# Kernel optimization log

Measured on AMD Instinct MI355X. Metric: run time of the kernel, lower is better.

Reference implementation:

```python
import jax, jax.numpy as jnp
import numpy as np
from jax import lax

FEAT = 192   # features
GROUP = 3
B, H, W = 16, 64, 64
CIN = 2 * FEAT        # 384, input channels of x
CGATE = 4 * FEAT      # 768, gate channels


def _group_ids(C, g=GROUP):
    # contiguous channel blocks: channel c -> group c*g//C
    return (np.arange(C) * g) // C


def _mask_B(out_c, in_c, kw):
    # PixelRNN mask 'B' for a (1,kw) kernel: left-of-center columns fully
    # connected, center column obeys group rule (out_group >= in_group),
    # right-of-center columns blocked.
    og = _group_ids(out_c)[:, None]
    ig = _group_ids(in_c)[None, :]
    center = (og >= ig).astype(np.float32)  # (out_c, in_c)
    m = np.zeros((out_c, in_c, 1, kw), dtype=np.float32)
    m[:, :, :, : kw // 2] = 1.0
    m[:, :, 0, kw // 2] = center
    return jnp.asarray(m)


def _shuffle(h):
    # (B, 3*4*(F/3), H, W): group-major gate layout -> gate-major group layout
    b, c, hh, ww = h.shape
    return h.reshape(b, GROUP, 4, FEAT // GROUP, hh, ww) \
            .transpose(0, 2, 1, 3, 4, 5).reshape(b, c, hh, ww)


def setup_inputs() -> dict:
    key = jax.random.key(0)
    k1, k2, k3, k4, k5 = jax.random.split(key, 5)
    x = jax.random.normal(k1, (B, CIN, H, W), dtype=jnp.float32)
    w_i2s = jax.random.normal(k2, (CGATE, CIN, 1, 3), dtype=jnp.float32) * 0.02
    w_s2s = jax.random.normal(k3, (CGATE, FEAT, 1, 3), dtype=jnp.float32) * 0.02
    w_skip = jax.random.normal(k4, (CIN, FEAT, 1, 1), dtype=jnp.float32) * 0.05
    b_skip = jax.random.normal(k5, (CIN,), dtype=jnp.float32) * 0.01
    return {"x": x, "w_i2s": w_i2s, "w_s2s": w_s2s,
            "w_skip": w_skip, "b_skip": b_skip}


def reference(x, w_i2s, w_s2s, w_skip, b_skip):
    mask_i2s = _mask_B(CGATE, CIN, 3)
    mask_skip = _mask_B(CIN, FEAT, 1)

    # input-to-state: masked (1,3) conv, 'same' padding on width
    h = lax.conv_general_dilated(
        x, w_i2s * mask_i2s, (1, 1), ((0, 0), (1, 1)),
        dimension_numbers=("NCHW", "OIHW", "NCHW"))
    h = _shuffle(h)                       # (B, 4F, H, W)

    w1 = w_s2s[:, :, 0, :]                # (4F, F, 3) for 1D width conv
    h_rows = h.transpose(2, 0, 1, 3)      # (H, B, 4F, W)

    def step(carry, h_row):
        _h, c = carry                     # each (B, F, W)
        s = lax.conv_general_dilated(
            _h, w1, (1,), ((1, 1),),
            dimension_numbers=("NCW", "OIW", "NCW")) + h_row
        o, f, i, g = jnp.split(jax.nn.sigmoid(s), 4, axis=1)
        c = f * c + i * g
        _h = o * jnp.tanh(c)
        return (_h, c), _h

    init = (jnp.zeros((B, FEAT, W), x.dtype), jnp.zeros((B, FEAT, W), x.dtype))
    _, out_h = lax.scan(step, init, h_rows)   # (H, B, F, W)
    out_h = out_h.transpose(1, 2, 0, 3)       # (B, F, H, W)

    skip = lax.conv_general_dilated(
        out_h, w_skip * mask_skip, (1, 1), ((0, 0), (0, 0)),
        dimension_numbers=("NCHW", "OIHW", "NCHW")) + b_skip[None, :, None, None]
    return x + skip
```

## Files before the change

kernel.cpp:

```cpp
#include <hip/hip_runtime.h>
#include <hip/hip_cooperative_groups.h>
#include <cmath>

#define FEAT  192
#define CINCH 384
#define CGATE 768
#define BATCH 16
#define HH    64
#define WW    64
#define NP    (BATCH*HH*WW)
#define KI2S  768
#define KS2S  576
#define NBLK  192
#define SCANT 512

using bf16   = __bf16;
using bf16x8 = __attribute__((ext_vector_type(8))) __bf16;
using bf16x4 = __attribute__((ext_vector_type(4))) __bf16;
using f32x4  = __attribute__((ext_vector_type(4))) float;
typedef unsigned long long u64;

__device__ __forceinline__ void ic_store64(u64* p, u64 v) {
    __hip_atomic_store(p, v, __ATOMIC_RELAXED, __HIP_MEMORY_SCOPE_AGENT);
}
__device__ __forceinline__ u64 ic_load64(const u64* p) {
    return __hip_atomic_load(p, __ATOMIC_RELAXED, __HIP_MEMORY_SCOPE_AGENT);
}
__device__ __forceinline__ void ic_store32(unsigned* p, unsigned v) {
    __hip_atomic_store(p, v, __ATOMIC_RELAXED, __HIP_MEMORY_SCOPE_AGENT);
}
__device__ __forceinline__ unsigned ic_load32(const unsigned* p) {
    return __hip_atomic_load(p, __ATOMIC_RELAXED, __HIP_MEMORY_SCOPE_AGENT);
}

__device__ __forceinline__ float sigm_fast(float v) {
    return __builtin_amdgcn_rcpf(1.f + __expf(-v));
}
__device__ __forceinline__ float tanh_fast(float v) {
    return 1.f - 2.f * __builtin_amdgcn_rcpf(1.f + __expf(2.f * v));
}

__global__ void pack_weights(const float* __restrict__ wi, const float* __restrict__ ws,
                             const float* __restrict__ wk,
                             bf16* __restrict__ WpA, bf16* __restrict__ WpS,
                             bf16* __restrict__ WpK) {
    int tid = blockIdx.x * 256 + threadIdx.x;
    int stride = gridDim.x * 256;
    for (int idx = tid; idx < CGATE * KI2S; idx += stride) {
        int cp = idx / KI2S, k = idx % KI2S;
        int q = cp / 192, r = cp % 192, g = r / 64, f = r % 64;
        int c = g * 256 + q * 64 + f;
        float v;
        if (k < CINCH) {
            v = wi[(c * CINCH + k) * 3 + 0];
        } else {
            int ic = k - CINCH;
            v = (g >= ic / 128) ? wi[(c * CINCH + ic) * 3 + 1] : 0.f;
        }
        WpA[idx] = (bf16)v;
    }
    for (int idx = tid; idx < CGATE * KS2S; idx += stride) {
        int oc = idx / KS2S, k = idx % KS2S;
        int t = k / FEAT, f = k % FEAT;
        WpS[idx] = (bf16)ws[(oc * FEAT + f) * 3 + t];
    }
    for (int idx = tid; idx < CINCH * FEAT; idx += stride) {
        int co = idx / FEAT, f = idx % FEAT;
        WpK[idx] = (co / 128 >= f / 64) ? (bf16)wk[idx] : (bf16)0.f;
    }
}

__global__ void pack_x(const float* __restrict__ x, bf16* __restrict__ Xp) {
    __shared__ float tile[64][65];
    int b = blockIdx.x >> 6, y = blockIdx.x & 63;
    const float* xb = x + ((size_t)b * CINCH * HH + y) * WW;
    bf16* Xrow = Xp + ((size_t)b * HH * WW + (size_t)y * WW) * KI2S;
    for (int ic0 = 0; ic0 < CINCH; ic0 += 64) {
        for (int rep = 0; rep < 16; ++rep) {
            int idx = rep * 256 + threadIdx.x;
            int i = idx >> 6, w = idx & 63;
            tile[i][w] = xb[(size_t)(ic0 + i) * (HH * WW) + w];
        }
        __syncthreads();
        for (int rep = 0; rep < 16; ++rep) {
            int idx = rep * 256 + threadIdx.x;
            int w = idx >> 6, i = idx & 63;
            Xrow[(size_t)w * KI2S + CINCH + ic0 + i] = (bf16)tile[i][w];
            Xrow[(size_t)w * KI2S + ic0 + i] = (w == 0) ? (bf16)0.f : (bf16)tile[i][w - 1];
        }
        __syncthreads();
    }
}

__global__ __launch_bounds__(256) void gemm_i2s(const bf16* __restrict__ A,
                                                const bf16* __restrict__ B,
                                                bf16* __restrict__ Hout) {
    __shared__ __align__(16) bf16 As[128 * 64];
    __shared__ __align__(16) bf16 Bs[128 * 64];
    const int m0 = blockIdx.y * 128;
    const int p0 = blockIdx.x * 128;
    const int tid = threadIdx.x;
    const int lane = tid & 63, wid = tid >> 6;
    const int quad = lane >> 4, col = lane & 15;
    const int mhalf = (wid & 1) * 64, nhalf = (wid >> 1) * 64;
    f32x4 acc[4][4] = {};
    for (int k0 = 0; k0 < KI2S; k0 += 64) {
        #pragma unroll
        for (int r = 0; r < 4; ++r) {
            int L = r * 256 + tid;
            int row = L >> 3, slot = L & 7;
            int c = slot ^ (row & 7);
            const bf16* srcA = &A[(size_t)(m0 + row) * KI2S + k0 + c * 8];
            const bf16* srcB = &B[(size_t)(p0 + row) * KI2S + k0 + c * 8];
            bf16* dstA = As + (size_t)(r * 256 + wid * 64) * 8;
            bf16* dstB = Bs + (size_t)(r * 256 + wid * 64) * 8;
            __builtin_amdgcn_global_load_lds(
                (const __attribute__((address_space(1))) void*)srcA,
                (__attribute__((address_space(3))) void*)dstA, 16, 0, 0);
            __builtin_amdgcn_global_load_lds(
                (const __attribute__((address_space(1))) void*)srcB,
                (__attribute__((address_space(3))) void*)dstB, 16, 0, 0);
        }
        __syncthreads();
        for (int kk = 0; kk < 2; ++kk) {
            bf16x8 af[4], bfv[4];
            for (int mt = 0; mt < 4; ++mt) {
                int row = mhalf + mt * 16 + col;
                int slot = (kk * 4 + quad) ^ (row & 7);
                af[mt] = *(const bf16x8*)(&As[row * 64 + slot * 8]);
            }
            for (int nt = 0; nt < 4; ++nt) {
                int row = nhalf + nt * 16 + col;
                int slot = (kk * 4 + quad) ^ (row & 7);
                bfv[nt] = *(const bf16x8*)(&Bs[row * 64 + slot * 8]);
            }
            for (int mt = 0; mt < 4; ++mt)
                for (int nt = 0; nt < 4; ++nt)
                    acc[mt][nt] = __builtin_amdgcn_mfma_f32_16x16x32_bf16(
                        af[mt], bfv[nt], acc[mt][nt], 0, 0, 0);
        }
        __syncthreads();
    }
    for (int mt = 0; mt < 4; ++mt)
        for (int nt = 0; nt < 4; ++nt) {
            int m = m0 + mhalf + mt * 16 + quad * 4;
            int p = p0 + nhalf + nt * 16 + col;
            for (int r = 0; r < 4; ++r)
                Hout[(size_t)(m + r) * NP + p] = (bf16)acc[mt][nt][r];
        }
}

__global__ __launch_bounds__(SCANT) void scan_kernel(
    const bf16* __restrict__ Hbuf,
    const bf16* __restrict__ Ws2s,
    const bf16* __restrict__ Wskip,
    const float* __restrict__ x,
    const float* __restrict__ b_skip,
    float* __restrict__ out,
    bf16* __restrict__ hg,
    unsigned* __restrict__ cnt) {
    cooperative_groups::grid_group grid = cooperative_groups::this_grid();
    __shared__ __align__(16) bf16 hlds[66 * 200];
    __shared__ __align__(16) bf16 hnew[64 * 20];
    const int bid = blockIdx.x;
    const int b = (bid & 7) * 2 + (bid / 96);
    const int j = (bid >> 3) % 12;
    const int tid = threadIdx.x, lane = tid & 63, wid = tid >> 6;
    const int quad = lane >> 4, col = lane & 15;
    const int wh = wid & 3;
    const int wn = wid >> 2;

    {
        const int total = 3 * 16 * 66 * 192 / 2;
        for (int i = bid * SCANT + tid; i < total; i += NBLK * SCANT)
            ((unsigned*)hg)[i] = 0u;
        if (tid < 32) cnt[(bid % 16) * 32 + tid] = 0u;
        for (int i = tid; i < 66 * 100; i += SCANT) ((unsigned*)hlds)[i] = 0u;
    }
    bf16x8 Ag[18];
    {
        int f = 16 * j + wh * 4 + (col >> 2), q = col & 3;
        const bf16* Arow = Ws2s + (size_t)(q * 192 + f) * KS2S + quad * 8;
        for (int kc = 0; kc < 18; ++kc) Ag[kc] = *(const bf16x8*)(Arow + kc * 32);
    }
    bf16x8 Ak[6];
    const int mtk = wid & 1, ntk = wid >> 1;
    {
        int co = 32 * j + mtk * 16 + col;
        const bf16* Krow = Wskip + (size_t)co * FEAT + quad * 8;
        for (int kc = 0; kc < 6; ++kc) Ak[kc] = *(const bf16x8*)(Krow + kc * 32);
    }
    const int fmine = 16 * j + wh * 4 + quad;
    const int lf = wh * 4 + quad;
    float cstate[2] = {0.f, 0.f};
    unsigned* myflags = cnt + b * 32;
    grid.sync();

    const size_t pbase = (size_t)b * HH * WW;
    float hadd[2][4];
    {
        for (int i = 0; i < 2; ++i) {
            int w = (wn * 2 + i) * 16 + col;
            for (int r = 0; r < 4; ++r)
                hadd[i][r] = (float)Hbuf[(size_t)(r * FEAT + fmine) * NP + pbase + w];
        }
    }

    for (int y = 0; y < 64; ++y) {
        f32x4 acc[2] = {};
        for (int kc = 0; kc < 18; ++kc) {
            int k0 = kc * 32 + quad * 8;
            int t = k0 / FEAT, f = k0 % FEAT;
            #pragma unroll
            for (int i = 0; i < 2; ++i) {
                int w = (wn * 2 + i) * 16 + col;
                bf16x8 bfr = *(const bf16x8*)(&hlds[(w + t) * 200 + f]);
                acc[i] = __builtin_amdgcn_mfma_f32_16x16x32_bf16(Ag[kc], bfr, acc[i], 0, 0, 0);
            }
        }
        #pragma unroll
        for (int i = 0; i < 2; ++i) {
            int w = (wn * 2 + i) * 16 + col;
            float so = acc[i][0] + hadd[i][0];
            float sf = acc[i][1] + hadd[i][1];
            float si = acc[i][2] + hadd[i][2];
            float sg = acc[i][3] + hadd[i][3];
            float go = sigm_fast(so);
            float gf = sigm_fast(sf);
            float gi = sigm_fast(si);
            float gg = sigm_fast(sg);
            float cc = gf * cstate[i] + gi * gg;
            cstate[i] = cc;
            hnew[w * 20 + lf] = (bf16)(go * tanh_fast(cc));
        }
        __syncthreads();

        if (tid < 256) {
            bf16* dst = hg + ((size_t)(y % 3) * 16 + b) * (66 * 192);
            int w = tid >> 2, fo = (tid & 3) * 4;
            u64 v = *(const u64*)(&hnew[w * 20 + fo]);
            ic_store64((u64*)(dst + (size_t)(w + 1) * 192 + 16 * j + fo), v);
        }
        __syncthreads();
        if (tid == 0) ic_store32(&myflags[j], (unsigned)(y + 1));

        if (y < 63) {
            const size_t prow = pbase + (size_t)(y + 1) * WW;
            #pragma unroll
            for (int i = 0; i < 2; ++i) {
                int w = (wn * 2 + i) * 16 + col;
                for (int r = 0; r < 4; ++r)
                    hadd[i][r] = (float)Hbuf[(size_t)(r * FEAT + fmine) * NP + prow + w];
            }
        }

        if (y > 0) {
            const int ym = y - 1;
            f32x4 acc2 = {};
            int wsk = ntk * 16 + col;
            for (int kc = 0; kc < 6; ++kc) {
                bf16x8 bfr = *(const bf16x8*)(&hlds[(wsk + 1) * 200 + kc * 32 + quad * 8]);
                acc2 = __builtin_amdgcn_mfma_f32_16x16x32_bf16(Ak[kc], bfr, acc2, 0, 0, 0);
            }
            for (int r = 0; r < 4; ++r) {
                int co = 32 * j + mtk * 16 + quad * 4 + r;
                size_t xi = ((size_t)(b * CINCH + co) * HH + ym) * WW + wsk;
                out[xi] = x[xi] + b_skip[co] + acc2[r];
            }
        }
        __syncthreads();

        {
            const unsigned tgt = (unsigned)(y + 1);
            while (true) {
                unsigned v = (lane < 12) ? ic_load32(&myflags[lane]) : tgt;
                if (__ballot(v >= tgt) == ~0ull) break;
                __builtin_amdgcn_s_sleep(1);
            }
            asm volatile("" ::: "memory");
        }

        {
            const u64* src = (const u64*)(hg + ((size_t)(y % 3) * 16 + b) * (66 * 192));
            #pragma unroll
            for (int it = 0; it < 7; ++it) {
                int c = it * SCANT + tid;
                if (c < 66 * 48) {
                    u64 v = ic_load64(src + c);
                    int w = c / 48, fc = c % 48;
                    *(u64*)(&hlds[w * 200 + fc * 4]) = v;
                }
            }
        }
        __syncthreads();
    }

    {
        f32x4 acc2 = {};
        int wsk = ntk * 16 + col;
        for (int kc = 0; kc < 6; ++kc) {
            bf16x8 bfr = *(const bf16x8*)(&hlds[(wsk + 1) * 200 + kc * 32 + quad * 8]);
            acc2 = __builtin_amdgcn_mfma_f32_16x16x32_bf16(Ak[kc], bfr, acc2, 0, 0, 0);
        }
        for (int r = 0; r < 4; ++r) {
            int co = 32 * j + mtk * 16 + quad * 4 + r;
            size_t xi = ((size_t)(b * CINCH + co) * HH + 63) * WW + wsk;
            out[xi] = x[xi] + b_skip[co] + acc2[r];
        }
    }
}

extern "C" void kernel_launch(void* const* d_in, const int* in_sizes, int n_in,
                              void* d_out, int out_size, void* d_ws, size_t ws_size,
                              hipStream_t stream) {
    const float* x      = (const float*)d_in[0];
    const float* w_i2s  = (const float*)d_in[1];
    const float* w_s2s  = (const float*)d_in[2];
    const float* w_skip = (const float*)d_in[3];
    const float* b_skip = (const float*)d_in[4];
    float* out = (float*)d_out;

    char* ws = (char*)d_ws;
    const size_t HBUF_B = (size_t)CGATE * NP * 2;
    bf16* Hbuf = (bf16*)ws;
    size_t off = HBUF_B;
    bf16* WpA  = (bf16*)(ws + off); off += (size_t)CGATE * KI2S * 2;
    bf16* WpS  = (bf16*)(ws + off); off += (size_t)CGATE * KS2S * 2;
    bf16* WpK  = (bf16*)(ws + off); off += (size_t)CINCH * FEAT * 2;
    bf16* hg   = (bf16*)(ws + off); off += (size_t)3 * 16 * 66 * 192 * 2;
    unsigned* cnt = (unsigned*)(ws + off);
    bf16* Xp   = (bf16*)d_out;

    pack_weights<<<256, 256, 0, stream>>>(w_i2s, w_s2s, w_skip, WpA, WpS, WpK);
    pack_x<<<BATCH * HH, 256, 0, stream>>>(x, Xp);
    dim3 g3(NP / 128, CGATE / 128);
    gemm_i2s<<<g3, 256, 0, stream>>>(WpA, Xp, Hbuf);

    void* args[] = { (void*)&Hbuf, (void*)&WpS, (void*)&WpK,
                     (void*)&x, (void*)&b_skip, (void*)&out, (void*)&hg, (void*)&cnt };
    hipLaunchCooperativeKernel((const void*)scan_kernel, dim3(NBLK), dim3(SCANT),
                               args, 0, stream);
}
```

Baseline: 666.5 us.

## Fuse input-to-state GEMM into the scan kernel with a row ring buffer

Removes the separate i2s GEMM kernel and its full-size H buffer. Each scan block now computes i2s GEMM tiles for future row pairs in slices interleaved with the recurrence steps, writes them to an 8-row ring buffer, and uses per-batch flags so consumers wait until their rows are ready. The shifted-x layout is no longer materialised; it is built at load time from a compact channel-last X plus a zero pad. This hides the GEMM behind the latency-bound scan and cuts DRAM traffic, but adds LDS pressure, extra syncthreads and spin-waits inside the serial loop, and strided 16-bit atomic stores.

Result: slower. 771.7 us (+15.8%).

```diff
diff --git a/kernel.cpp b/kernel.cpp
--- a/kernel.cpp
+++ b/kernel.cpp
@@ -32,6 +32,15 @@
 __device__ __forceinline__ unsigned ic_load32(const unsigned* p) {
     return __hip_atomic_load(p, __ATOMIC_RELAXED, __HIP_MEMORY_SCOPE_AGENT);
 }
+__device__ __forceinline__ void ic_store16(bf16* p, bf16 h) {
+    union { bf16 h; unsigned short u; } cv; cv.h = h;
+    __hip_atomic_store((unsigned short*)p, cv.u, __ATOMIC_RELAXED, __HIP_MEMORY_SCOPE_AGENT);
+}
+__device__ __forceinline__ float ic_load_bf16(const bf16* p) {
+    union { unsigned short u; bf16 h; } cv;
+    cv.u = __hip_atomic_load((const unsigned short*)p, __ATOMIC_RELAXED, __HIP_MEMORY_SCOPE_AGENT);
+    return (float)cv.h;
+}
 
 __device__ __forceinline__ float sigm_fast(float v) {
     return __builtin_amdgcn_rcpf(1.f + __expf(-v));
@@ -43,9 +52,10 @@
 __global__ void pack_weights(const float* __restrict__ wi, const float* __restrict__ ws,
                              const float* __restrict__ wk,
                              bf16* __restrict__ WpA, bf16* __restrict__ WpS,
-                             bf16* __restrict__ WpK) {
+                             bf16* __restrict__ WpK, bf16* __restrict__ zp) {
     int tid = blockIdx.x * 256 + threadIdx.x;
     int stride = gridDim.x * 256;
+    for (int idx = tid; idx < 512; idx += stride) zp[idx] = (bf16)0.f;
     for (int idx = tid; idx < CGATE * KI2S; idx += stride) {
         int cp = idx / KI2S, k = idx % KI2S;
         int q = cp / 192, r = cp % 192, g = r / 64, f = r % 64;
@@ -70,11 +80,11 @@
     }
 }
 
-__global__ void pack_x(const float* __restrict__ x, bf16* __restrict__ Xp) {
+__global__ void pack_xc(const float* __restrict__ x, bf16* __restrict__ Xc) {
     __shared__ float tile[64][65];
     int b = blockIdx.x >> 6, y = blockIdx.x & 63;
     const float* xb = x + ((size_t)b * CINCH * HH + y) * WW;
-    bf16* Xrow = Xp + ((size_t)b * HH * WW + (size_t)y * WW) * KI2S;
+    bf16* Xrow = Xc + (size_t)((b * HH + y) * WW) * CINCH;
     for (int ic0 = 0; ic0 < CINCH; ic0 += 64) {
         for (int rep = 0; rep < 16; ++rep) {
             int idx = rep * 256 + threadIdx.x;
@@ -85,83 +95,29 @@
         for (int rep = 0; rep < 16; ++rep) {
             int idx = rep * 256 + threadIdx.x;
             int w = idx >> 6, i = idx & 63;
-            Xrow[(size_t)w * KI2S + CINCH + ic0 + i] = (bf16)tile[i][w];
-            Xrow[(size_t)w * KI2S + ic0 + i] = (w == 0) ? (bf16)0.f : (bf16)tile[i][w - 1];
-        }
-        __syncthreads();
-    }
-}
-
-__global__ __launch_bounds__(256) void gemm_i2s(const bf16* __restrict__ A,
-                                                const bf16* __restrict__ B,
-                                                bf16* __restrict__ Hout) {
-    __shared__ __align__(16) bf16 As[128 * 64];
-    __shared__ __align__(16) bf16 Bs[128 * 64];
-    const int m0 = blockIdx.y * 128;
-    const int p0 = blockIdx.x * 128;
-    const int tid = threadIdx.x;
-    const int lane = tid & 63, wid = tid >> 6;
-    const int quad = lane >> 4, col = lane & 15;
-    const int mhalf = (wid & 1) * 64, nhalf = (wid >> 1) * 64;
-    f32x4 acc[4][4] = {};
-    for (int k0 = 0; k0 < KI2S; k0 += 64) {
-        #pragma unroll
-        for (int r = 0; r < 4; ++r) {
-            int L = r * 256 + tid;
-            int row = L >> 3, slot = L & 7;
-            int c = slot ^ (row & 7);
-            const bf16* srcA = &A[(size_t)(m0 + row) * KI2S + k0 + c * 8];
-            const bf16* srcB = &B[(size_t)(p0 + row) * KI2S + k0 + c * 8];
-            bf16* dstA = As + (size_t)(r * 256 + wid * 64) * 8;
-            bf16* dstB = Bs + (size_t)(r * 256 + wid * 64) * 8;
-            __builtin_amdgcn_global_load_lds(
-                (const __attribute__((address_space(1))) void*)srcA,
-                (__attribute__((address_space(3))) void*)dstA, 16, 0, 0);
-            __builtin_amdgcn_global_load_lds(
-                (const __attribute__((address_space(1))) void*)srcB,
-                (__attribute__((address_space(3))) void*)dstB, 16, 0, 0);
-        }
-        __syncthreads();
-        for (int kk = 0; kk < 2; ++kk) {
-            bf16x8 af[4], bfv[4];
-            for (int mt = 0; mt < 4; ++mt) {
-                int row = mhalf + mt * 16 + col;
-                int slot = (kk * 4 + quad) ^ (row & 7);
-                af[mt] = *(const bf16x8*)(&As[row * 64 + slot * 8]);
-            }
-            for (int nt = 0; nt < 4; ++nt) {
-                int row = nhalf + nt * 16 + col;
-                int slot = (kk * 4 + quad) ^ (row & 7);
-                bfv[nt] = *(const bf16x8*)(&Bs[row * 64 + slot * 8]);
-            }
-            for (int mt = 0; mt < 4; ++mt)
-                for (int nt = 0; nt < 4; ++nt)
-                    acc[mt][nt] = __builtin_amdgcn_mfma_f32_16x16x32_bf16(
-                        af[mt], bfv[nt], acc[mt][nt], 0, 0, 0);
-        }
-        __syncthreads();
-    }
-    for (int mt = 0; mt < 4; ++mt)
-        for (int nt = 0; nt < 4; ++nt) {
-            int m = m0 + mhalf + mt * 16 + quad * 4;
-            int p = p0 + nhalf + nt * 16 + col;
-            for (int r = 0; r < 4; ++r)
-                Hout[(size_t)(m + r) * NP + p] = (bf16)acc[mt][nt][r];
-        }
-}
-
-__global__ __launch_bounds__(SCANT) void scan_kernel(
-    const bf16* __restrict__ Hbuf,
+            Xrow[(size_t)w * CINCH + ic0 + i] = (bf16)tile[i][w];
+        }
+        __syncthreads();
+    }
+}
+
+__global__ __launch_bounds__(SCANT, 2) void scan_kernel(
+    const bf16* __restrict__ WpA,
     const bf16* __restrict__ Ws2s,
     const bf16* __restrict__ Wskip,
+    const bf16* __restrict__ Xc,
+    const bf16* __restrict__ zp,
     const float* __restrict__ x,
     const float* __restrict__ b_skip,
     float* __restrict__ out,
     bf16* __restrict__ hg,
-    unsigned* __restrict__ cnt) {
+    unsigned* __restrict__ cnt,
+    bf16* __restrict__ Hring) {
     cooperative_groups::grid_group grid = cooperative_groups::this_grid();
     __shared__ __align__(16) bf16 hlds[66 * 200];
     __shared__ __align__(16) bf16 hnew[64 * 20];
+    __shared__ __align__(16) bf16 As2[128 * 64];
+    __shared__ __align__(16) bf16 Bs2[128 * 64];
     const int bid = blockIdx.x;
     const int b = (bid & 7) * 2 + (bid / 96);
     const int j = (bid >> 3) % 12;
@@ -169,12 +125,14 @@
     const int quad = lane >> 4, col = lane & 15;
     const int wh = wid & 3;
     const int wn = wid >> 2;
+    const int mq = wid & 1, nq = wid >> 1;
 
     {
         const int total = 3 * 16 * 66 * 192 / 2;
         for (int i = bid * SCANT + tid; i < total; i += NBLK * SCANT)
             ((unsigned*)hg)[i] = 0u;
         if (tid < 32) cnt[(bid % 16) * 32 + tid] = 0u;
+        if (tid >= 64 && tid < 96) cnt[512 + (bid % 16) * 32 + (tid - 64)] = 0u;
         for (int i = tid; i < 66 * 100; i += SCANT) ((unsigned*)hlds)[i] = 0u;
     }
     bf16x8 Ag[18];
@@ -194,16 +152,113 @@
     const int lf = wh * 4 + quad;
     float cstate[2] = {0.f, 0.f};
     unsigned* myflags = cnt + b * 32;
+    unsigned* gflags  = cnt + 512 + b * 32;
     grid.sync();
 
-    const size_t pbase = (size_t)b * HH * WW;
+#define GSTAGE(M0, P0, K0) do {                                                    \
+    _Pragma("unroll")                                                              \
+    for (int r_ = 0; r_ < 2; ++r_) {                                               \
+        int L_ = r_ * 512 + tid;                                                   \
+        int row_ = L_ >> 3, slot_ = L_ & 7;                                        \
+        int c_ = slot_ ^ (row_ & 7);                                               \
+        const bf16* srcA = &WpA[(size_t)((M0) + row_) * KI2S + (K0) + c_ * 8];     \
+        const bf16* srcB;                                                          \
+        if ((K0) < 384) {                                                          \
+            srcB = ((row_ & 63) == 0) ? (zp + c_ * 8)                              \
+                 : &Xc[(size_t)((P0) + row_ - 1) * CINCH + (K0) + c_ * 8];         \
+        } else {                                                                   \
+            srcB = &Xc[(size_t)((P0) + row_) * CINCH + (K0) - 384 + c_ * 8];       \
+        }                                                                          \
+        bf16* dA = As2 + (size_t)(r_ * 512 + wid * 64) * 8;                        \
+        bf16* dB = Bs2 + (size_t)(r_ * 512 + wid * 64) * 8;                        \
+        __builtin_amdgcn_global_load_lds(                                          \
+            (const __attribute__((address_space(1))) void*)srcA,                   \
+            (__attribute__((address_space(3))) void*)dA, 16, 0, 0);                \
+        __builtin_amdgcn_global_load_lds(                                          \
+            (const __attribute__((address_space(1))) void*)srcB,                   \
+            (__attribute__((address_space(3))) void*)dB, 16, 0, 0);                \
+    }                                                                              \
+} while (0)
+
+#define GMFMA(ACC) do {                                                            \
+    _Pragma("unroll")                                                              \
+    for (int kk_ = 0; kk_ < 2; ++kk_) {                                            \
+        bf16x8 af_[4], bv_[2];                                                     \
+        _Pragma("unroll")                                                          \
+        for (int mt_ = 0; mt_ < 4; ++mt_) {                                        \
+            int row_ = mq * 64 + mt_ * 16 + col;                                   \
+            int slot_ = (kk_ * 4 + quad) ^ (row_ & 7);                             \
+            af_[mt_] = *(const bf16x8*)(&As2[row_ * 64 + slot_ * 8]);              \
+        }                                                                          \
+        _Pragma("unroll")                                                          \
+        for (int nt_ = 0; nt_ < 2; ++nt_) {                                        \
+            int row_ = nq * 32 + nt_ * 16 + col;                                   \
+            int slot_ = (kk_ * 4 + quad) ^ (row_ & 7);                             \
+            bv_[nt_] = *(const bf16x8*)(&Bs2[row_ * 64 + slot_ * 8]);              \
+        }                                                                          \
+        _Pragma("unroll")                                                          \
+        for (int mt_ = 0; mt_ < 4; ++mt_)                                          \
+            _Pragma("unroll")                                                      \
+            for (int nt_ = 0; nt_ < 2; ++nt_)                                      \
+                ACC[mt_][nt_] = __builtin_amdgcn_mfma_f32_16x16x32_bf16(           \
+                    af_[mt_], bv_[nt_], ACC[mt_][nt_], 0, 0, 0);                   \
+    }                                                                              \
+} while (0)
+
+#define GEPI(ACC, M0, YH) do {                                                     \
+    _Pragma("unroll")                                                              \
+    for (int mt_ = 0; mt_ < 4; ++mt_)                                              \
+        _Pragma("unroll")                                                          \
+        for (int nt_ = 0; nt_ < 2; ++nt_) {                                        \
+            int m_ = (M0) + mq * 64 + mt_ * 16 + quad * 4;                         \
+            int idx_ = nq * 32 + nt_ * 16 + col;                                   \
+            int yy_ = (YH) * 2 + (idx_ >> 6), wl_ = idx_ & 63;                     \
+            _Pragma("unroll")                                                      \
+            for (int r_ = 0; r_ < 4; ++r_)                                         \
+                ic_store16(&Hring[(((size_t)(m_ + r_) * 16 + b) * 8 +              \
+                                   (yy_ & 7)) * 64 + wl_],                         \
+                           (bf16)ACC[mt_][nt_][r_]);                               \
+        }                                                                          \
+} while (0)
+
+#define HPREF(YY) do {                                                             \
+    int slot_ = (YY) & 7;                                                          \
+    _Pragma("unroll")                                                              \
+    for (int i_ = 0; i_ < 2; ++i_) {                                               \
+        int w_ = (wn * 2 + i_) * 16 + col;                                         \
+        _Pragma("unroll")                                                          \
+        for (int r_ = 0; r_ < 4; ++r_)                                             \
+            hadd[i_][r_] = ic_load_bf16(&Hring[(((size_t)(r_ * FEAT + fmine) * 16  \
+                                                 + b) * 8 + slot_) * 64 + w_]);    \
+    }                                                                              \
+} while (0)
+
+    f32x4 accg[4][2];
     float hadd[2][4];
+
     {
-        for (int i = 0; i < 2; ++i) {
-            int w = (wn * 2 + i) * 16 + col;
-            for (int r = 0; r < 4; ++r)
-                hadd[i][r] = (float)Hbuf[(size_t)(r * FEAT + fmine) * NP + pbase + w];
-        }
+        const int t0 = j;
+        const int m0_ = (t0 % 6) * 128, yh_ = t0 / 6;
+        const size_t p0_ = ((size_t)b * 64 + yh_ * 2) * 64;
+        #pragma unroll
+        for (int mt_ = 0; mt_ < 4; ++mt_)
+            for (int nt_ = 0; nt_ < 2; ++nt_) accg[mt_][nt_] = f32x4{0.f, 0.f, 0.f, 0.f};
+        for (int ki = 0; ki < 12; ++ki) {
+            GSTAGE(m0_, p0_, ki * 64);
+            __syncthreads();
+            GMFMA(accg);
+            __syncthreads();
+        }
+        GEPI(accg, m0_, yh_);
+        __syncthreads();
+        if (tid == 0) ic_store32(&gflags[j], 1u);
+        while (true) {
+            unsigned v = (lane < 12) ? ic_load32(&gflags[lane]) : 1u;
+            if (__ballot(v >= 1u) == ~0ull) break;
+            __builtin_amdgcn_s_sleep(1);
+        }
+        asm volatile("" ::: "memory");
+        HPREF(0);
     }
 
     for (int y = 0; y < 64; ++y) {
@@ -244,14 +299,44 @@
         __syncthreads();
         if (tid == 0) ic_store32(&myflags[j], (unsigned)(y + 1));
 
+        if (y < 60) {
+            const int n_ = (y >> 2) + 1;
+            const int t_ = j + 12 * n_;
+            const int m0_ = (t_ % 6) * 128, yh_ = t_ / 6;
+            const size_t p0_ = ((size_t)b * 64 + yh_ * 2) * 64;
+            const int ph_ = y & 3;
+            if (ph_ == 0) {
+                #pragma unroll
+                for (int mt_ = 0; mt_ < 4; ++mt_)
+                    for (int nt_ = 0; nt_ < 2; ++nt_) accg[mt_][nt_] = f32x4{0.f, 0.f, 0.f, 0.f};
+            }
+            for (int ki = ph_ * 3; ki < ph_ * 3 + 3; ++ki) {
+                GSTAGE(m0_, p0_, ki * 64);
+                __syncthreads();
+                GMFMA(accg);
+                __syncthreads();
+            }
+            if (ph_ == 3) {
+                GEPI(accg, m0_, yh_);
+                __syncthreads();
+                if (tid == 0) ic_store32(&gflags[j], (unsigned)(n_ + 1));
+            }
+        }
+
         if (y < 63) {
-            const size_t prow = pbase + (size_t)(y + 1) * WW;
-            #pragma unroll
-            for (int i = 0; i < 2; ++i) {
-                int w = (wn * 2 + i) * 16 + col;
-                for (int r = 0; r < 4; ++r)
-                    hadd[i][r] = (float)Hbuf[(size_t)(r * FEAT + fmine) * NP + prow + w];
-            }
+            const int yhreq = (y + 1) >> 1;
+            unsigned tgt = 0;
+            if (lane < 12) {
+                int o = (lane >= 6) ? 1 : 0;
+                tgt = (yhreq >= o) ? (unsigned)(((yhreq - o) >> 1) + 1) : 0u;
+            }
+            while (true) {
+                unsigned v = (lane < 12) ? ic_load32(&gflags[lane]) : 0u;
+                if (__ballot(v >= tgt) == ~0ull) break;
+                __builtin_amdgcn_s_sleep(1);
+            }
+            asm volatile("" ::: "memory");
+            HPREF(y + 1);
         }
 
         if (y > 0) {
@@ -308,6 +393,11 @@
             out[xi] = x[xi] + b_skip[co] + acc2[r];
         }
     }
+
+#undef GSTAGE
+#undef GMFMA
+#undef GEPI
+#undef HPREF
 }
 
 extern "C" void kernel_launch(void* const* d_in, const int* in_sizes, int n_in,
@@ -321,23 +411,22 @@
     float* out = (float*)d_out;
 
     char* ws = (char*)d_ws;
-    const size_t HBUF_B = (size_t)CGATE * NP * 2;
-    bf16* Hbuf = (bf16*)ws;
-    size_t off = HBUF_B;
-    bf16* WpA  = (bf16*)(ws + off); off += (size_t)CGATE * KI2S * 2;
-    bf16* WpS  = (bf16*)(ws + off); off += (size_t)CGATE * KS2S * 2;
-    bf16* WpK  = (bf16*)(ws + off); off += (size_t)CINCH * FEAT * 2;
-    bf16* hg   = (bf16*)(ws + off); off += (size_t)3 * 16 * 66 * 192 * 2;
-    unsigned* cnt = (unsigned*)(ws + off);
-    bf16* Xp   = (bf16*)d_out;
-
-    pack_weights<<<256, 256, 0, stream>>>(w_i2s, w_s2s, w_skip, WpA, WpS, WpK);
-    pack_x<<<BATCH * HH, 256, 0, stream>>>(x, Xp);
-    dim3 g3(NP / 128, CGATE / 128);
-    gemm_i2s<<<g3, 256, 0, stream>>>(WpA, Xp, Hbuf);
-
-    void* args[] = { (void*)&Hbuf, (void*)&WpS, (void*)&WpK,
-                     (void*)&x, (void*)&b_skip, (void*)&out, (void*)&hg, (void*)&cnt };
+    bf16* Xc    = (bf16*)ws;
+    size_t off  = (size_t)NP * CINCH * 2;
+    bf16* WpA   = (bf16*)(ws + off); off += (size_t)CGATE * KI2S * 2;
+    bf16* WpS   = (bf16*)(ws + off); off += (size_t)CGATE * KS2S * 2;
+    bf16* WpK   = (bf16*)(ws + off); off += (size_t)CINCH * FEAT * 2;
+    bf16* hg    = (bf16*)(ws + off); off += (size_t)3 * 16 * 66 * 192 * 2;
+    bf16* Hring = (bf16*)(ws + off); off += (size_t)CGATE * 16 * 8 * 64 * 2;
+    unsigned* cnt = (unsigned*)(ws + off); off += 4096;
+    bf16* zp    = (bf16*)(ws + off); off += 1024;
+
+    pack_weights<<<256, 256, 0, stream>>>(w_i2s, w_s2s, w_skip, WpA, WpS, WpK, zp);
+    pack_xc<<<BATCH * HH, 256, 0, stream>>>(x, Xc);
+
+    void* args[] = { (void*)&WpA, (void*)&WpS, (void*)&WpK, (void*)&Xc, (void*)&zp,
+                     (void*)&x, (void*)&b_skip, (void*)&out, (void*)&hg, (void*)&cnt,
+                     (void*)&Hring };
     hipLaunchCooperativeKernel((const void*)scan_kernel, dim3(NBLK), dim3(SCANT),
                                args, 0, stream);
 }
```
